# Kernel tuning notes

Measured on AMD Instinct MI355X. Metric: run time of the kernel, lower is better.

The kernel has to match this reference:

```python
import jax, jax.numpy as jnp
import numpy as np

B, C, F, H, W = 2, 512, 8, 32, 32


def setup_inputs() -> dict:
    key = jax.random.key(0)
    ks = jax.random.split(key, 10)
    s = 0.02
    return {
        "x": jax.random.normal(ks[0], (B, C, F, H, W), jnp.float32),
        "gamma": jnp.ones((C, 1, 1, 1), jnp.float32),
        "wq": jax.random.normal(ks[1], (C, C), jnp.float32) * s,
        "bq": jnp.zeros((C,), jnp.float32),
        "wk": jax.random.normal(ks[2], (C, C), jnp.float32) * s,
        "bk": jnp.zeros((C,), jnp.float32),
        "wv": jax.random.normal(ks[3], (C, C), jnp.float32) * s,
        "bv": jnp.zeros((C,), jnp.float32),
        "wo": jax.random.normal(ks[4], (C, C), jnp.float32) * s,
        "bo": jnp.zeros((C,), jnp.float32),
    }


def _rms_norm(x, gamma):
    # F.normalize(x, dim=1) * sqrt(C) * gamma  (channel-first, eps=1e-12)
    n = jnp.sqrt(jnp.sum(x * x, axis=1, keepdims=True))
    return x / jnp.maximum(n, 1e-12) * (x.shape[1] ** 0.5) * gamma


def _conv1x1(x, w, b):
    # 1x1x1 Conv3d == per-voxel linear over channels
    return jnp.einsum("oi,bifhw->bofhw", w, x) + b[None, :, None, None, None]


def reference(x, gamma, wq, bq, wk, bk, wv, bv, wo, bo):
    b, c, f, h, w = x.shape
    n_hw = h * w
    S = f * n_hw

    hn = _rms_norm(x, gamma)
    q = _conv1x1(hn, wq, bq).reshape(b, c, S).swapaxes(1, 2)  # [b, S, c]
    k = _conv1x1(hn, wk, bk).reshape(b, c, S).swapaxes(1, 2)
    v = _conv1x1(hn, wv, bv).reshape(b, c, S).swapaxes(1, 2)

    # block-causal mask: query attends to all tokens in frames <= its own frame
    frame_id = jnp.arange(S) // n_hw
    allow = frame_id[:, None] >= frame_id[None, :]  # [S, S] bool

    scores = jnp.einsum("bsc,btc->bst", q, k) / jnp.sqrt(jnp.asarray(c, x.dtype))
    scores = jnp.where(allow[None], scores, -jnp.inf)
    p = jax.nn.softmax(scores, axis=-1)
    o = jnp.einsum("bst,btc->bsc", p, v)  # [b, S, c]

    o = o.swapaxes(1, 2).reshape(b, c, f, h, w)
    return x + _conv1x1(o, wo, bo)
```

## Files before the change

kernel.cpp:

```cpp
#include <hip/hip_runtime.h>
#include <hip/hip_bf16.h>
#include <math.h>

typedef __bf16 bf16;
typedef __bf16 bf16x8 __attribute__((ext_vector_type(8)));
typedef float f32x4 __attribute__((ext_vector_type(4)));

#define C_DIM 512
#define S_DIM 8192

__device__ __forceinline__ void async_ld16(const void* g, void* l) {
    __builtin_amdgcn_global_load_lds(
        (const __attribute__((address_space(1))) unsigned int*)g,
        (__attribute__((address_space(3))) unsigned int*)l, 16, 0, 0);
}

__device__ __forceinline__ unsigned char to_fp8(float v) {
    return (unsigned char)(__builtin_amdgcn_cvt_pk_fp8_f32(v, v, 0, false) & 0xFF);
}

__global__ void detect_kernel(const unsigned short* __restrict__ xu, int* __restrict__ flag) {
    int j = threadIdx.x;
    for (int i = 16 + j; i < 320; i += 64) flag[i] = 0;
    unsigned e = (xu[2 * j] >> 7) & 0xFF;
    unsigned long long m = __ballot(e >= 90 && e <= 140);
    if (j == 0) *flag = (__popcll(m) >= 48) ? 1 : 0;
}

__global__ __launch_bounds__(256) void convert_kernel(const void* __restrict__ s0,
                                                      const void* __restrict__ s1,
                                                      const void* __restrict__ s2,
                                                      const void* __restrict__ s3,
                                                      bf16* __restrict__ dst,
                                                      const int* __restrict__ flag) {
    int y = blockIdx.y;
    const void* srcs[4] = {s0, s1, s2, s3};
    const void* src = srcs[y];
    int i = blockIdx.x * 256 + threadIdx.x;
    bf16* d = dst + (size_t)y * 262144;
    if (*flag) {
        volatile const bf16* s = (volatile const bf16*)src;
        d[i] = s[i];
    } else {
        volatile const float* s = (volatile const float*)src;
        d[i] = (bf16)s[i];
    }
}

__global__ __launch_bounds__(256) void rms_kernel(const void* __restrict__ x,
                                                  float* __restrict__ r,
                                                  const int* __restrict__ flag) {
    __shared__ float red[4][64];
    int b  = blockIdx.x >> 7;
    int s0 = (blockIdx.x & 127) * 64;
    int sl = threadIdx.x & 63;
    int cq = threadIdx.x >> 6;
    float acc = 0.f;
    if (*flag) {
        const bf16* xp = (const bf16*)x + ((size_t)b * C_DIM + cq * 128) * S_DIM + s0 + sl;
        for (int c = 0; c < 128; ++c) { float v = (float)xp[(size_t)c * S_DIM]; acc += v * v; }
    } else {
        const float* xp = (const float*)x + ((size_t)b * C_DIM + cq * 128) * S_DIM + s0 + sl;
        for (int c = 0; c < 128; ++c) { float v = xp[(size_t)c * S_DIM]; acc += v * v; }
    }
    red[cq][sl] = acc;
    __syncthreads();
    if (cq == 0) {
        float t = red[0][sl] + red[1][sl] + red[2][sl] + red[3][sl];
        r[b * S_DIM + s0 + sl] = 22.627416997969522f / fmaxf(sqrtf(t), 1e-12f);
    }
}

__global__ __launch_bounds__(256) void hn_kernel(const void* __restrict__ x,
                                                 const void* __restrict__ gamma,
                                                 const float* __restrict__ r,
                                                 bf16* __restrict__ hn,
                                                 const int* __restrict__ flag) {
    __shared__ float tile[64][65];
    int f  = *flag;
    int b  = blockIdx.z;
    int c0 = blockIdx.y * 64;
    int s0 = blockIdx.x * 64;
    int col = threadIdx.x & 63;
    int row = threadIdx.x >> 6;
    if (f) {
        const bf16* xp = (const bf16*)x + ((size_t)b * C_DIM + c0) * S_DIM + s0;
        for (int i = 0; i < 16; ++i)
            tile[row + i * 4][col] = (float)xp[(size_t)(row + i * 4) * S_DIM + col];
    } else {
        const float* xp = (const float*)x + ((size_t)b * C_DIM + c0) * S_DIM + s0;
        for (int i = 0; i < 16; ++i)
            tile[row + i * 4][col] = xp[(size_t)(row + i * 4) * S_DIM + col];
    }
    __syncthreads();
    float g;
    if (f) g = (float)((const bf16*)gamma)[c0 + col];
    else   g = ((const float*)gamma)[c0 + col];
    bf16* hp = hn + ((size_t)b * S_DIM + s0) * C_DIM + c0;
    for (int i = 0; i < 16; ++i) {
        int s_l = row + i * 4;
        float rv = r[b * S_DIM + s0 + s_l];
        hp[(size_t)s_l * C_DIM + col] = (bf16)(tile[col][s_l] * rv * g);
    }
}

__global__ __launch_bounds__(256, 2) void gemm_kernel(const bf16* __restrict__ A,
                                                      const bf16* __restrict__ W,
                                                      const void* __restrict__ bias,
                                                      const void* __restrict__ resid,
                                                      void* __restrict__ out,
                                                      int mode,
                                                      const int* __restrict__ flag) {
    __shared__ bf16 As[128 * 40];
    __shared__ bf16 Bs[128 * 40];
    int f  = *flag;
    int m0 = blockIdx.x * 128;
    int n0 = blockIdx.y * 128;
    int tid  = threadIdx.x;
    int lane = tid & 63;
    int wave = tid >> 6;
    int wm = (wave & 1) * 64;
    int wn = (wave >> 1) * 64;
    int l15  = lane & 15;
    int quad = lane >> 4;

    f32x4 acc[4][4] = {};
    for (int k0 = 0; k0 < C_DIM; k0 += 32) {
        __syncthreads();
        for (int u = tid; u < 512; u += 256) {
            int rrow = u >> 2;
            int cc = (u & 3) * 8;
            *(bf16x8*)&As[rrow * 40 + cc] =
                *(const bf16x8*)&A[(size_t)(m0 + rrow) * C_DIM + k0 + cc];
            *(bf16x8*)&Bs[rrow * 40 + cc] =
                *(const bf16x8*)&W[(size_t)(n0 + rrow) * C_DIM + k0 + cc];
        }
        __syncthreads();
        bf16x8 af[4], bfr[4];
#pragma unroll
        for (int i = 0; i < 4; ++i)
            af[i] = *(bf16x8*)&As[(wm + i * 16 + l15) * 40 + quad * 8];
#pragma unroll
        for (int j = 0; j < 4; ++j)
            bfr[j] = *(bf16x8*)&Bs[(wn + j * 16 + l15) * 40 + quad * 8];
#pragma unroll
        for (int i = 0; i < 4; ++i)
#pragma unroll
            for (int j = 0; j < 4; ++j)
                acc[i][j] = __builtin_amdgcn_mfma_f32_16x16x32_bf16(af[i], bfr[j], acc[i][j], 0, 0, 0);
    }
    if (mode == 0) {
        unsigned char* op = (unsigned char*)out;
#pragma unroll
        for (int i = 0; i < 4; ++i)
#pragma unroll
            for (int j = 0; j < 4; ++j)
#pragma unroll
                for (int rg = 0; rg < 4; ++rg) {
                    int m = m0 + wm + i * 16 + quad * 4 + rg;
                    int n = n0 + wn + j * 16 + l15;
                    float bv = f ? (float)((const bf16*)bias)[n] : ((const float*)bias)[n];
                    op[(size_t)m * C_DIM + n] = to_fp8(acc[i][j][rg] + bv);
                }
    } else if (mode == 3) {
        unsigned char* op = (unsigned char*)out;
#pragma unroll
        for (int i = 0; i < 4; ++i)
#pragma unroll
            for (int j = 0; j < 4; ++j)
#pragma unroll
                for (int rg = 0; rg < 4; ++rg) {
                    int m = m0 + wm + i * 16 + quad * 4 + rg;
                    int n = n0 + wn + j * 16 + l15;
                    float bv = f ? (float)((const bf16*)bias)[n] : ((const float*)bias)[n];
                    size_t idx = ((((size_t)(m >> 5) * 64 + (n >> 3)) * 32 + (m & 31)) * 8) + (n & 7);
                    op[idx] = to_fp8(acc[i][j][rg] + bv);
                }
    } else if (mode == 1) {
        unsigned char* op = (unsigned char*)out;
#pragma unroll
        for (int i = 0; i < 4; ++i)
#pragma unroll
            for (int j = 0; j < 4; ++j)
#pragma unroll
                for (int rg = 0; rg < 4; ++rg) {
                    int m = m0 + wm + i * 16 + quad * 4 + rg;
                    int n = n0 + wn + j * 16 + l15;
                    float bv = f ? (float)((const bf16*)bias)[n] : ((const float*)bias)[n];
                    size_t idx = ((((size_t)(m >> 5) * 4 + ((m >> 3) & 3)) * 512 + n) * 8) + (m & 7);
                    op[idx] = to_fp8(acc[i][j][rg] + bv);
                }
    } else if (f) {
        bf16* op = (bf16*)out;
        const bf16* rp = (const bf16*)resid;
#pragma unroll
        for (int i = 0; i < 4; ++i)
#pragma unroll
            for (int j = 0; j < 4; ++j)
#pragma unroll
                for (int rg = 0; rg < 4; ++rg) {
                    int m = m0 + wm + i * 16 + quad * 4 + rg;
                    int n = n0 + wn + j * 16 + l15;
                    float bv = (float)((const bf16*)bias)[n];
                    int b = m >> 13, s = m & 8191;
                    size_t idx = ((size_t)b * C_DIM + n) * S_DIM + s;
                    op[idx] = (bf16)(acc[i][j][rg] + bv + (float)rp[idx]);
                }
    } else {
        float* op = (float*)out;
        const float* rp = (const float*)resid;
#pragma unroll
        for (int i = 0; i < 4; ++i)
#pragma unroll
            for (int j = 0; j < 4; ++j)
#pragma unroll
                for (int rg = 0; rg < 4; ++rg) {
                    int m = m0 + wm + i * 16 + quad * 4 + rg;
                    int n = n0 + wn + j * 16 + l15;
                    float bv = ((const float*)bias)[n];
                    int b = m >> 13, s = m & 8191;
                    size_t idx = ((size_t)b * C_DIM + n) * S_DIM + s;
                    op[idx] = acc[i][j][rg] + bv + rp[idx];
                }
    }
}

__global__ __launch_bounds__(256, 2) void attn_split_kernel(const unsigned char* __restrict__ q,
                                                            const unsigned char* __restrict__ k,
                                                            const unsigned char* __restrict__ vt,
                                                            bf16* __restrict__ part,
                                                            float* __restrict__ lsum,
                                                            int* __restrict__ counter,
                                                            int* __restrict__ cnt,
                                                            int* __restrict__ slist) {
    __shared__ unsigned char Ks[2][16384];
    __shared__ unsigned char Vs[2][16384];
    __shared__ unsigned char Ps[4][16 * 40];
    __shared__ int slot_sh;
    int tid  = threadIdx.x;
    int lane = tid & 63;
    int wave = tid >> 6;
    int l15  = lane & 15;
    int quad = lane >> 4;

    int g0 = blockIdx.x * 72;
    int b_ = (g0 >= 18432) ? 1 : 0;
    int r  = g0 - b_ * 18432;
    int f_ = 0;
    while (r >= 256 * (f_ + 1) * (f_ + 2)) ++f_;
    int L   = 32 * (f_ + 1);
    int rr  = r - 256 * f_ * (f_ + 1);
    int tif = rr / L;
    int cw  = rr - tif * L;

    long qf[16];
    {
        int qbase = (f_ * 16 + tif) * 64 + wave * 16;
        const unsigned char* qp = q + (size_t)(b_ * S_DIM + qbase + l15) * C_DIM;
#pragma unroll
        for (int ks = 0; ks < 16; ++ks)
            qf[ks] = *(const long*)&qp[ks * 32 + quad * 8];
    }

    f32x4 oacc[32] = {};
    float l_i[4] = {0.f, 0.f, 0.f, 0.f};
    const float scale = 0.044194173824159216f;

    {
        const unsigned char* ka = k  + ((size_t)(b_ * 256 + cw) << 14);
        const unsigned char* va = vt + ((size_t)(b_ * 256 + cw) << 14);
#pragma unroll
        for (int j = 0; j < 4; ++j) {
            int base = (j * 4 + wave) * 1024;
            async_ld16(ka + base + lane * 16, &Ks[0][base]);
            async_ld16(va + base + lane * 16, &Vs[0][base]);
        }
    }
    __syncthreads();

    for (int i = 0; i < 72; ++i) {
        int last = (i == 71);
        int nb = b_, nf = f_, nL = L, ntif = tif, ncw = cw + 1;
        int newtile = 0;
        if (ncw == L) {
            ncw = 0; newtile = 1; ntif = tif + 1;
            if (ntif == 16) {
                ntif = 0; nf = f_ + 1; nL = L + 32;
                if (nf == 8) { nf = 0; nL = 32; nb = b_ + 1; }
            }
        }
        if (last) { nb = b_; nf = f_; nL = L; ntif = tif; ncw = cw; newtile = 0; }

        {
            const unsigned char* ka = k  + ((size_t)(nb * 256 + ncw) << 14);
            const unsigned char* va = vt + ((size_t)(nb * 256 + ncw) << 14);
            unsigned char* kd = Ks[(i + 1) & 1];
            unsigned char* vd = Vs[(i + 1) & 1];
#pragma unroll
            for (int j = 0; j < 4; ++j) {
                int base = (j * 4 + wave) * 1024;
                async_ld16(ka + base + lane * 16, kd + base);
                async_ld16(va + base + lane * 16, vd + base);
            }
        }
        const unsigned char* kb = Ks[i & 1];
        const unsigned char* vb = Vs[i & 1];
        f32x4 st[2] = {};
#pragma unroll
        for (int nt = 0; nt < 2; ++nt) {
#pragma unroll
            for (int ks = 0; ks < 16; ++ks) {
                long kf = *(const long*)&kb[(ks * 4 + quad) * 256 + (nt * 16 + l15) * 8];
                st[nt] = __builtin_amdgcn_mfma_f32_16x16x32_fp8_fp8(qf[ks], kf, st[nt], 0, 0, 0);
            }
        }
        float p0[4], p1[4];
#pragma unroll
        for (int rg = 0; rg < 4; ++rg) {
            p0[rg] = __expf(st[0][rg] * scale);
            p1[rg] = __expf(st[1][rg] * scale);
            l_i[rg] += p0[rg] + p1[rg];
        }
        unsigned char* pw = Ps[wave];
#pragma unroll
        for (int rg = 0; rg < 4; ++rg) {
            pw[(quad * 4 + rg) * 40 + l15] = to_fp8(p0[rg]);
            pw[(quad * 4 + rg) * 40 + 16 + l15] = to_fp8(p1[rg]);
        }
        long pf = *(const long*)&pw[l15 * 40 + quad * 8];
#pragma unroll
        for (int dn = 0; dn < 32; ++dn) {
            long vf = *(const long*)&vb[quad * 4096 + (dn * 16 + l15) * 8];
            oacc[dn] = __builtin_amdgcn_mfma_f32_16x16x32_fp8_fp8(pf, vf, oacc[dn], 0, 0, 0);
        }

        if (last || newtile) {
            int ord = b_ * 128 + f_ * 16 + tif;
            if (tid == 0) {
                int s = atomicAdd(counter, 1);
                int pos = atomicAdd(&cnt[ord], 1);
                slist[ord * 8 + pos] = s;
                slot_sh = s;
            }
            __syncthreads();
            int slot = slot_sh;
#pragma unroll
            for (int rg = 0; rg < 4; ++rg)
                for (int d = 1; d < 16; d <<= 1)
                    l_i[rg] += __shfl_xor(l_i[rg], d);
            float rinv[4];
#pragma unroll
            for (int rg = 0; rg < 4; ++rg) rinv[rg] = 1.f / l_i[rg];
            bf16* pp = part + ((size_t)slot * 64 + wave * 16) * C_DIM;
#pragma unroll
            for (int dn = 0; dn < 32; ++dn)
#pragma unroll
                for (int rg = 0; rg < 4; ++rg)
                    pp[(size_t)(quad * 4 + rg) * C_DIM + dn * 16 + l15] =
                        (bf16)(oacc[dn][rg] * rinv[rg]);
            if (l15 == 0) {
#pragma unroll
                for (int rg = 0; rg < 4; ++rg)
                    lsum[slot * 64 + wave * 16 + quad * 4 + rg] = l_i[rg];
            }
            if (!last) {
#pragma unroll
                for (int dn = 0; dn < 32; ++dn) oacc[dn] = (f32x4){0.f, 0.f, 0.f, 0.f};
#pragma unroll
                for (int rg = 0; rg < 4; ++rg) l_i[rg] = 0.f;
                int nqbase = (nf * 16 + ntif) * 64 + wave * 16;
                const unsigned char* qp = q + (size_t)(nb * S_DIM + nqbase + l15) * C_DIM;
#pragma unroll
                for (int ks = 0; ks < 16; ++ks)
                    qf[ks] = *(const long*)&qp[ks * 32 + quad * 8];
            }
        }
        b_ = nb; f_ = nf; L = nL; tif = ntif; cw = ncw;
        __syncthreads();
    }
}

__global__ __launch_bounds__(256, 2) void attn_kernel(const unsigned char* __restrict__ q,
                                                      const unsigned char* __restrict__ k,
                                                      const unsigned char* __restrict__ vt,
                                                      bf16* __restrict__ ob) {
    __shared__ unsigned char Ks[2][16384];
    __shared__ unsigned char Vs[2][16384];
    __shared__ unsigned char Ps[4][16 * 40];
    int id = blockIdx.x;
    int b = id >> 7;
    int t = id & 127;
    int q0 = t * 64;
    int kc0 = 0;
    int kc1 = ((t >> 4) + 1) << 10;
    int tid  = threadIdx.x;
    int lane = tid & 63;
    int wave = tid >> 6;
    int l15  = lane & 15;
    int quad = lane >> 4;
    int qbase = q0 + wave * 16;
    int nchunks = (kc1 - kc0) >> 5;

    long qf[16];
    const unsigned char* qp = q + (size_t)(b * S_DIM + qbase + l15) * C_DIM;
#pragma unroll
    for (int ks = 0; ks < 16; ++ks)
        qf[ks] = *(const long*)&qp[ks * 32 + quad * 8];

    f32x4 oacc[32] = {};
    float l_i[4] = {0.f, 0.f, 0.f, 0.f};
    const float scale = 0.044194173824159216f;

    const unsigned char* kbase = k  + ((size_t)(b * 256 + (kc0 >> 5)) << 14);
    const unsigned char* vbase = vt + ((size_t)(b * 256 + (kc0 >> 5)) << 14);

#pragma unroll
    for (int j = 0; j < 4; ++j) {
        int base = (j * 4 + wave) * 1024;
        async_ld16(kbase + base + lane * 16, &Ks[0][base]);
        async_ld16(vbase + base + lane * 16, &Vs[0][base]);
    }
    __syncthreads();

    for (int p = 0; p < nchunks; ++p) {
        int pn = (p + 1 < nchunks) ? (p + 1) : p;
        const unsigned char* ksub = kbase + ((size_t)pn << 14);
        const unsigned char* vsub = vbase + ((size_t)pn << 14);
        unsigned char* kd = Ks[(p + 1) & 1];
        unsigned char* vd = Vs[(p + 1) & 1];
#pragma unroll
        for (int j = 0; j < 4; ++j) {
            int base = (j * 4 + wave) * 1024;
            async_ld16(ksub + base + lane * 16, kd + base);
            async_ld16(vsub + base + lane * 16, vd + base);
        }
        const unsigned char* kb = Ks[p & 1];
        const unsigned char* vb = Vs[p & 1];
        f32x4 st[2] = {};
#pragma unroll
        for (int nt = 0; nt < 2; ++nt) {
#pragma unroll
            for (int ks = 0; ks < 16; ++ks) {
                long kf = *(const long*)&kb[(ks * 4 + quad) * 256 + (nt * 16 + l15) * 8];
                st[nt] = __builtin_amdgcn_mfma_f32_16x16x32_fp8_fp8(qf[ks], kf, st[nt], 0, 0, 0);
            }
        }
        float p0[4], p1[4];
#pragma unroll
        for (int rg = 0; rg < 4; ++rg) {
            p0[rg] = __expf(st[0][rg] * scale);
            p1[rg] = __expf(st[1][rg] * scale);
            l_i[rg] += p0[rg] + p1[rg];
        }
        unsigned char* pw = Ps[wave];
#pragma unroll
        for (int rg = 0; rg < 4; ++rg) {
            pw[(quad * 4 + rg) * 40 + l15] = to_fp8(p0[rg]);
            pw[(quad * 4 + rg) * 40 + 16 + l15] = to_fp8(p1[rg]);
        }
        long pf = *(const long*)&pw[l15 * 40 + quad * 8];
#pragma unroll
        for (int dn = 0; dn < 32; ++dn) {
            long vf = *(const long*)&vb[quad * 4096 + (dn * 16 + l15) * 8];
            oacc[dn] = __builtin_amdgcn_mfma_f32_16x16x32_fp8_fp8(pf, vf, oacc[dn], 0, 0, 0);
        }
        __syncthreads();
    }
#pragma unroll
    for (int rg = 0; rg < 4; ++rg)
        for (int d = 1; d < 16; d <<= 1)
            l_i[rg] += __shfl_xor(l_i[rg], d);
    float rinv[4];
#pragma unroll
    for (int rg = 0; rg < 4; ++rg) rinv[rg] = 1.f / l_i[rg];
    bf16* op = ob + (size_t)(b * S_DIM + qbase) * C_DIM;
#pragma unroll
    for (int dn = 0; dn < 32; ++dn)
#pragma unroll
        for (int rg = 0; rg < 4; ++rg)
            op[(size_t)(quad * 4 + rg) * C_DIM + dn * 16 + l15] =
                (bf16)(oacc[dn][rg] * rinv[rg]);
}

__global__ __launch_bounds__(256) void combine_kernel(const bf16* __restrict__ part,
                                                      const float* __restrict__ lsum,
                                                      bf16* __restrict__ ob,
                                                      const int* __restrict__ cnt,
                                                      const int* __restrict__ slist) {
    int id = blockIdx.x;
    int b  = id >> 7;
    int q0 = (id & 127) * 64;
    int U  = cnt[id];
    int qq = threadIdx.x >> 2;
    int cr = threadIdx.x & 3;
    int sl[8];
    float w[8];
    float D = 0.f;
    for (int u = 0; u < U; ++u) {
        sl[u] = slist[id * 8 + u];
        w[u] = lsum[sl[u] * 64 + qq];
        D += w[u];
    }
    float Dinv = 1.f / D;
    for (int u = 0; u < U; ++u) w[u] *= Dinv;
    bf16* op = ob + (size_t)(b * S_DIM + q0 + qq) * C_DIM + cr * 128;
    for (int ch = 0; ch < 16; ++ch) {
        float acc[8] = {};
        for (int u = 0; u < U; ++u) {
            bf16x8 pv = *(const bf16x8*)&part[((size_t)sl[u] * 64 + qq) * C_DIM + cr * 128 + ch * 8];
#pragma unroll
            for (int j = 0; j < 8; ++j) acc[j] += w[u] * (float)pv[j];
        }
        bf16x8 o8;
#pragma unroll
        for (int j = 0; j < 8; ++j) o8[j] = (bf16)acc[j];
        *(bf16x8*)&op[ch * 8] = o8;
    }
}

extern "C" void kernel_launch(void* const* d_in, const int* in_sizes, int n_in,
                              void* d_out, int out_size, void* d_ws, size_t ws_size,
                              hipStream_t stream) {
    const void* x     = d_in[0];
    const void* gamma = d_in[1];
    const void* wq    = d_in[2];
    const void* bq    = d_in[3];
    const void* wk    = d_in[4];
    const void* bk    = d_in[5];
    const void* wv    = d_in[6];
    const void* bv    = d_in[7];
    const void* wo    = d_in[8];
    const void* bo    = d_in[9];

    char* ws = (char*)d_ws;
    int*   flag    = (int*)ws;
    int*   counter = (int*)(ws + 64);
    int*   cntp    = (int*)(ws + 256);
    int*   slist   = (int*)(ws + 0x12000);
    float* r_buf   = (float*)(ws + 4096);
    bf16* wqb = (bf16*)(ws + 0x20000);
    bf16* wkb = (bf16*)(ws + 0xA0000);
    bf16* wvb = (bf16*)(ws + 0x120000);
    bf16* wob = (bf16*)(ws + 0x1A0000);
    float* lsum_buf = (float*)(ws + 0x240000);
    bf16* hn  = (bf16*)(ws + 0x400000);
    unsigned char* qb  = (unsigned char*)(ws + 0x1400000);
    unsigned char* kb  = (unsigned char*)(ws + 0x1C00000);
    unsigned char* vtb = (unsigned char*)(ws + 0x2400000);
    bf16* ob  = (bf16*)(ws + 0x2C00000);
    bf16* part = (bf16*)(ws + 0x5400000);

    const size_t ws_needed_split = 0x5400000ull + 768ull * 64 * 512 * 2;
    int split = (ws_size >= ws_needed_split) ? 1 : 0;

    hipLaunchKernelGGL(detect_kernel, dim3(1), dim3(64), 0, stream,
                       (const unsigned short*)x, flag);
    hipLaunchKernelGGL(convert_kernel, dim3(1024, 4), dim3(256), 0, stream,
                       wq, wk, wv, wo, wqb, flag);
    hipLaunchKernelGGL(rms_kernel, dim3(256), dim3(256), 0, stream, x, r_buf, flag);
    hipLaunchKernelGGL(hn_kernel, dim3(128, 8, 2), dim3(256), 0, stream, x, gamma, r_buf, hn, flag);
    hipLaunchKernelGGL(gemm_kernel, dim3(128, 4), dim3(256), 0, stream, hn, wqb, bq, (const void*)nullptr, qb, 0, flag);
    hipLaunchKernelGGL(gemm_kernel, dim3(128, 4), dim3(256), 0, stream, hn, wkb, bk, (const void*)nullptr, kb, 3, flag);
    hipLaunchKernelGGL(gemm_kernel, dim3(128, 4), dim3(256), 0, stream, hn, wvb, bv, (const void*)nullptr, vtb, 1, flag);
    if (split) {
        hipLaunchKernelGGL(attn_split_kernel, dim3(512), dim3(256), 0, stream,
                           qb, kb, vtb, part, lsum_buf, counter, cntp, slist);
        hipLaunchKernelGGL(combine_kernel, dim3(256), dim3(256), 0, stream,
                           part, lsum_buf, ob, cntp, slist);
    } else {
        hipLaunchKernelGGL(attn_kernel, dim3(256), dim3(256), 0, stream, qb, kb, vtb, ob);
    }
    hipLaunchKernelGGL(gemm_kernel, dim3(128, 4), dim3(256), 0, stream, ob, wob, bo, x, d_out, 2, flag);
}
```

Before: 427.3 us.

## Share K/V chunks across two query tiles per block with triple-buffered staging

The split attention kernel now runs 512-thread blocks in which two groups of four waves process paired query tiles (p and p+8 within a frame). Each staged K/V chunk is therefore reused by twice as many queries, halving the global K/V traffic per unit of work. Staging becomes a three-deep ring with an explicit vmcnt wait and barrier, so loads run two chunks ahead. The QK^T MFMA chain is also split into two independent accumulators to cut dependency stalls. In exchange LDS use per block grows and each flush writes two slots, which could lower occupancy.

```diff
diff --git a/kernel.cpp b/kernel.cpp
--- a/kernel.cpp
+++ b/kernel.cpp
@@ -225,7 +225,7 @@
     }
 }
 
-__global__ __launch_bounds__(256, 2) void attn_split_kernel(const unsigned char* __restrict__ q,
+__global__ __launch_bounds__(512, 2) void attn_split_kernel(const unsigned char* __restrict__ q,
                                                             const unsigned char* __restrict__ k,
                                                             const unsigned char* __restrict__ vt,
                                                             bf16* __restrict__ part,
@@ -233,30 +233,45 @@
                                                             int* __restrict__ counter,
                                                             int* __restrict__ cnt,
                                                             int* __restrict__ slist) {
-    __shared__ unsigned char Ks[2][16384];
-    __shared__ unsigned char Vs[2][16384];
-    __shared__ unsigned char Ps[4][16 * 40];
+    __shared__ unsigned char Ks[3][16384];
+    __shared__ unsigned char Vs[3][16384];
+    __shared__ unsigned char Ps[8][16 * 40];
     __shared__ int slot_sh;
     int tid  = threadIdx.x;
     int lane = tid & 63;
     int wave = tid >> 6;
+    int qgrp = wave >> 2;
+    int w4   = wave & 3;
     int l15  = lane & 15;
     int quad = lane >> 4;
 
     int g0 = blockIdx.x * 72;
-    int b_ = (g0 >= 18432) ? 1 : 0;
-    int r  = g0 - b_ * 18432;
-    int f_ = 0;
-    while (r >= 256 * (f_ + 1) * (f_ + 2)) ++f_;
-    int L   = 32 * (f_ + 1);
-    int rr  = r - 256 * f_ * (f_ + 1);
-    int tif = rr / L;
-    int cw  = rr - tif * L;
+    int b0 = (g0 >= 9216) ? 1 : 0;
+    int r  = g0 - b0 * 9216;
+    int f0 = 0;
+    while (r >= 128 * (f0 + 1) * (f0 + 2)) ++f0;
+    int L0  = 32 * (f0 + 1);
+    int rr  = r - 128 * f0 * (f0 + 1);
+    int p0  = rr / L0;
+    int c0  = rr - p0 * L0;
+
+    auto adv = [](int& b, int& f, int& p, int& c, int& L) {
+        if (++c == L) {
+            c = 0;
+            if (++p == 8) {
+                p = 0;
+                if (++f == 8) { f = 0; L = 32; ++b; }
+                else L += 32;
+            }
+        }
+    };
+    int b1 = b0, f1 = f0, p1 = p0, c1 = c0, L1 = L0; adv(b1, f1, p1, c1, L1);
+    int b2 = b1, f2 = f1, p2 = p1, c2 = c1, L2 = L1; adv(b2, f2, p2, c2, L2);
 
     long qf[16];
     {
-        int qbase = (f_ * 16 + tif) * 64 + wave * 16;
-        const unsigned char* qp = q + (size_t)(b_ * S_DIM + qbase + l15) * C_DIM;
+        int qbase = (f0 * 16 + p0 + qgrp * 8) * 64 + w4 * 16;
+        const unsigned char* qp = q + (size_t)(b0 * S_DIM + qbase + l15) * C_DIM;
 #pragma unroll
         for (int ks = 0; ks < 16; ++ks)
             qf[ks] = *(const long*)&qp[ks * 32 + quad * 8];
@@ -266,66 +281,105 @@
     float l_i[4] = {0.f, 0.f, 0.f, 0.f};
     const float scale = 0.044194173824159216f;
 
-    {
-        const unsigned char* ka = k  + ((size_t)(b_ * 256 + cw) << 14);
-        const unsigned char* va = vt + ((size_t)(b_ * 256 + cw) << 14);
-#pragma unroll
-        for (int j = 0; j < 4; ++j) {
-            int base = (j * 4 + wave) * 1024;
-            async_ld16(ka + base + lane * 16, &Ks[0][base]);
-            async_ld16(va + base + lane * 16, &Vs[0][base]);
-        }
-    }
-    __syncthreads();
-
+    auto stage = [&](int buf, int sb, int sc) {
+        const unsigned char* kc = k  + ((size_t)(sb * 256 + sc) << 14);
+        const unsigned char* vc = vt + ((size_t)(sb * 256 + sc) << 14);
+#pragma unroll
+        for (int j = 0; j < 2; ++j) {
+            int off = wave * 2048 + j * 1024;
+            async_ld16(kc + off + lane * 16, &Ks[buf][off]);
+            async_ld16(vc + off + lane * 16, &Vs[buf][off]);
+        }
+    };
+
+    auto do_flush = [&](int fb, int ff, int fp) {
+        int ordA = fb * 128 + ff * 16 + fp;
+        if (tid == 0) {
+            int s = atomicAdd(counter, 2);
+            int posA = atomicAdd(&cnt[ordA], 1);
+            slist[ordA * 8 + posA] = s;
+            int posB = atomicAdd(&cnt[ordA + 8], 1);
+            slist[(ordA + 8) * 8 + posB] = s + 1;
+            slot_sh = s;
+        }
+        __syncthreads();
+        int slot = slot_sh + qgrp;
+        float ls[4];
+#pragma unroll
+        for (int rg = 0; rg < 4; ++rg) {
+            float v = l_i[rg];
+            for (int d = 1; d < 16; d <<= 1) v += __shfl_xor(v, d);
+            ls[rg] = v;
+        }
+        float rinv[4];
+#pragma unroll
+        for (int rg = 0; rg < 4; ++rg) rinv[rg] = 1.f / ls[rg];
+        bf16* ppd = part + ((size_t)slot * 64 + w4 * 16) * C_DIM;
+#pragma unroll
+        for (int dn = 0; dn < 32; ++dn)
+#pragma unroll
+            for (int rg = 0; rg < 4; ++rg)
+                ppd[(size_t)(quad * 4 + rg) * C_DIM + dn * 16 + l15] =
+                    (bf16)(oacc[dn][rg] * rinv[rg]);
+        if (l15 == 0) {
+#pragma unroll
+            for (int rg = 0; rg < 4; ++rg)
+                lsum[slot * 64 + w4 * 16 + quad * 4 + rg] = ls[rg];
+        }
+    };
+
+    stage(0, b0, c0);
+    stage(1, b1, c1);
+    __builtin_amdgcn_sched_barrier(0);
+    asm volatile("s_waitcnt vmcnt(4)" ::: "memory");
+    __builtin_amdgcn_s_barrier();
+    __builtin_amdgcn_sched_barrier(0);
+
+    int pb = b0, pfr = f0, ppr = p0;
     for (int i = 0; i < 72; ++i) {
-        int last = (i == 71);
-        int nb = b_, nf = f_, nL = L, ntif = tif, ncw = cw + 1;
-        int newtile = 0;
-        if (ncw == L) {
-            ncw = 0; newtile = 1; ntif = tif + 1;
-            if (ntif == 16) {
-                ntif = 0; nf = f_ + 1; nL = L + 32;
-                if (nf == 8) { nf = 0; nL = 32; nb = b_ + 1; }
+        if (i > 0 && (p0 != ppr || f0 != pfr || b0 != pb)) {
+            do_flush(pb, pfr, ppr);
+#pragma unroll
+            for (int dn = 0; dn < 32; ++dn) oacc[dn] = (f32x4){0.f, 0.f, 0.f, 0.f};
+#pragma unroll
+            for (int rg = 0; rg < 4; ++rg) l_i[rg] = 0.f;
+            int qbase = (f0 * 16 + p0 + qgrp * 8) * 64 + w4 * 16;
+            const unsigned char* qp = q + (size_t)(b0 * S_DIM + qbase + l15) * C_DIM;
+#pragma unroll
+            for (int ks = 0; ks < 16; ++ks)
+                qf[ks] = *(const long*)&qp[ks * 32 + quad * 8];
+        }
+        pb = b0; pfr = f0; ppr = p0;
+
+        int bc = i % 3;
+        int bp = bc + 2; if (bp >= 3) bp -= 3;
+        stage(bp, b2, c2);
+
+        const unsigned char* kb = Ks[bc];
+        const unsigned char* vb = Vs[bc];
+        f32x4 stA[2] = {}, stB[2] = {};
+#pragma unroll
+        for (int nt = 0; nt < 2; ++nt) {
+#pragma unroll
+            for (int ks = 0; ks < 8; ++ks) {
+                long kfa = *(const long*)&kb[(ks * 4 + quad) * 256 + (nt * 16 + l15) * 8];
+                stA[nt] = __builtin_amdgcn_mfma_f32_16x16x32_fp8_fp8(qf[ks], kfa, stA[nt], 0, 0, 0);
+                long kfb = *(const long*)&kb[((ks + 8) * 4 + quad) * 256 + (nt * 16 + l15) * 8];
+                stB[nt] = __builtin_amdgcn_mfma_f32_16x16x32_fp8_fp8(qf[ks + 8], kfb, stB[nt], 0, 0, 0);
             }
         }
-        if (last) { nb = b_; nf = f_; nL = L; ntif = tif; ncw = cw; newtile = 0; }
-
-        {
-            const unsigned char* ka = k  + ((size_t)(nb * 256 + ncw) << 14);
-            const unsigned char* va = vt + ((size_t)(nb * 256 + ncw) << 14);
-            unsigned char* kd = Ks[(i + 1) & 1];
-            unsigned char* vd = Vs[(i + 1) & 1];
-#pragma unroll
-            for (int j = 0; j < 4; ++j) {
-                int base = (j * 4 + wave) * 1024;
-                async_ld16(ka + base + lane * 16, kd + base);
-                async_ld16(va + base + lane * 16, vd + base);
-            }
-        }
-        const unsigned char* kb = Ks[i & 1];
-        const unsigned char* vb = Vs[i & 1];
-        f32x4 st[2] = {};
-#pragma unroll
-        for (int nt = 0; nt < 2; ++nt) {
-#pragma unroll
-            for (int ks = 0; ks < 16; ++ks) {
-                long kf = *(const long*)&kb[(ks * 4 + quad) * 256 + (nt * 16 + l15) * 8];
-                st[nt] = __builtin_amdgcn_mfma_f32_16x16x32_fp8_fp8(qf[ks], kf, st[nt], 0, 0, 0);
-            }
-        }
-        float p0[4], p1[4];
+        float p0v[4], p1v[4];
 #pragma unroll
         for (int rg = 0; rg < 4; ++rg) {
-            p0[rg] = __expf(st[0][rg] * scale);
-            p1[rg] = __expf(st[1][rg] * scale);
-            l_i[rg] += p0[rg] + p1[rg];
+            p0v[rg] = __expf((stA[0][rg] + stB[0][rg]) * scale);
+            p1v[rg] = __expf((stA[1][rg] + stB[1][rg]) * scale);
+            l_i[rg] += p0v[rg] + p1v[rg];
         }
         unsigned char* pw = Ps[wave];
 #pragma unroll
         for (int rg = 0; rg < 4; ++rg) {
-            pw[(quad * 4 + rg) * 40 + l15] = to_fp8(p0[rg]);
-            pw[(quad * 4 + rg) * 40 + 16 + l15] = to_fp8(p1[rg]);
+            pw[(quad * 4 + rg) * 40 + l15] = to_fp8(p0v[rg]);
+            pw[(quad * 4 + rg) * 40 + 16 + l15] = to_fp8(p1v[rg]);
         }
         long pf = *(const long*)&pw[l15 * 40 + quad * 8];
 #pragma unroll
@@ -334,50 +388,16 @@
             oacc[dn] = __builtin_amdgcn_mfma_f32_16x16x32_fp8_fp8(pf, vf, oacc[dn], 0, 0, 0);
         }
 
-        if (last || newtile) {
-            int ord = b_ * 128 + f_ * 16 + tif;
-            if (tid == 0) {
-                int s = atomicAdd(counter, 1);
-                int pos = atomicAdd(&cnt[ord], 1);
-                slist[ord * 8 + pos] = s;
-                slot_sh = s;
-            }
-            __syncthreads();
-            int slot = slot_sh;
-#pragma unroll
-            for (int rg = 0; rg < 4; ++rg)
-                for (int d = 1; d < 16; d <<= 1)
-                    l_i[rg] += __shfl_xor(l_i[rg], d);
-            float rinv[4];
-#pragma unroll
-            for (int rg = 0; rg < 4; ++rg) rinv[rg] = 1.f / l_i[rg];
-            bf16* pp = part + ((size_t)slot * 64 + wave * 16) * C_DIM;
-#pragma unroll
-            for (int dn = 0; dn < 32; ++dn)
-#pragma unroll
-                for (int rg = 0; rg < 4; ++rg)
-                    pp[(size_t)(quad * 4 + rg) * C_DIM + dn * 16 + l15] =
-                        (bf16)(oacc[dn][rg] * rinv[rg]);
-            if (l15 == 0) {
-#pragma unroll
-                for (int rg = 0; rg < 4; ++rg)
-                    lsum[slot * 64 + wave * 16 + quad * 4 + rg] = l_i[rg];
-            }
-            if (!last) {
-#pragma unroll
-                for (int dn = 0; dn < 32; ++dn) oacc[dn] = (f32x4){0.f, 0.f, 0.f, 0.f};
-#pragma unroll
-                for (int rg = 0; rg < 4; ++rg) l_i[rg] = 0.f;
-                int nqbase = (nf * 16 + ntif) * 64 + wave * 16;
-                const unsigned char* qp = q + (size_t)(nb * S_DIM + nqbase + l15) * C_DIM;
-#pragma unroll
-                for (int ks = 0; ks < 16; ++ks)
-                    qf[ks] = *(const long*)&qp[ks * 32 + quad * 8];
-            }
-        }
-        b_ = nb; f_ = nf; L = nL; tif = ntif; cw = ncw;
-        __syncthreads();
-    }
+        b0 = b1; f0 = f1; p0 = p1; c0 = c1; L0 = L1;
+        b1 = b2; f1 = f2; p1 = p2; c1 = c2; L1 = L2;
+        if (g0 + i + 3 < 18432) adv(b2, f2, p2, c2, L2);
+
+        __builtin_amdgcn_sched_barrier(0);
+        asm volatile("s_waitcnt vmcnt(4)" ::: "memory");
+        __builtin_amdgcn_s_barrier();
+        __builtin_amdgcn_sched_barrier(0);
+    }
+    do_flush(pb, pfr, ppr);
 }
 
 __global__ __launch_bounds__(256, 2) void attn_kernel(const unsigned char* __restrict__ q,
@@ -391,7 +411,6 @@
     int b = id >> 7;
     int t = id & 127;
     int q0 = t * 64;
-    int kc0 = 0;
     int kc1 = ((t >> 4) + 1) << 10;
     int tid  = threadIdx.x;
     int lane = tid & 63;
@@ -399,7 +418,7 @@
     int l15  = lane & 15;
     int quad = lane >> 4;
     int qbase = q0 + wave * 16;
-    int nchunks = (kc1 - kc0) >> 5;
+    int nchunks = kc1 >> 5;
 
     long qf[16];
     const unsigned char* qp = q + (size_t)(b * S_DIM + qbase + l15) * C_DIM;
@@ -411,8 +430,8 @@
     float l_i[4] = {0.f, 0.f, 0.f, 0.f};
     const float scale = 0.044194173824159216f;
 
-    const unsigned char* kbase = k  + ((size_t)(b * 256 + (kc0 >> 5)) << 14);
-    const unsigned char* vbase = vt + ((size_t)(b * 256 + (kc0 >> 5)) << 14);
+    const unsigned char* kbase = k  + ((size_t)(b * 256) << 14);
+    const unsigned char* vbase = vt + ((size_t)(b * 256) << 14);
 
 #pragma unroll
     for (int j = 0; j < 4; ++j) {
@@ -563,7 +582,7 @@
     hipLaunchKernelGGL(gemm_kernel, dim3(128, 4), dim3(256), 0, stream, hn, wkb, bk, (const void*)nullptr, kb, 3, flag);
     hipLaunchKernelGGL(gemm_kernel, dim3(128, 4), dim3(256), 0, stream, hn, wvb, bv, (const void*)nullptr, vtb, 1, flag);
     if (split) {
-        hipLaunchKernelGGL(attn_split_kernel, dim3(512), dim3(256), 0, stream,
+        hipLaunchKernelGGL(attn_split_kernel, dim3(256), dim3(512), 0, stream,
                            qb, kb, vtb, part, lsum_buf, counter, cntp, slist);
         hipLaunchKernelGGL(combine_kernel, dim3(256), dim3(256), 0, stream,
                            part, lsum_buf, ob, cntp, slist);
```

Result: slower. 446.0 us (+4.4%).
